# Performance work log

Hardware: AMD Instinct MI355X
Metric: run time of the kernel (lower is better)

The kernel has to match this reference:

```python
import jax, jax.numpy as jnp
import numpy as np

N_NODES = 50000
N_EDGES = 800000
IN_F = 128
OUT_F = 128
EDGE_F = 6


def setup_inputs() -> dict:
    key = jax.random.key(0)
    k1, k2, k3, k4, k5, k6, k7 = jax.random.split(key, 7)
    nodeFeatures = jax.random.normal(k1, (N_NODES, IN_F), dtype=jnp.float32)
    edgeIndex = jax.random.randint(k2, (N_EDGES, 2), 0, N_NODES, dtype=jnp.int64)
    edgeFeatures = jax.random.normal(k3, (N_EDGES, EDGE_F), dtype=jnp.float32)
    # nn.Linear params (kaiming-uniform-ish init scale)
    lim_n = 1.0 / np.sqrt(IN_F)
    lim_e = 1.0 / np.sqrt(EDGE_F)
    W = jax.random.uniform(k4, (IN_F, OUT_F), minval=-lim_n, maxval=lim_n, dtype=jnp.float32)
    b = jax.random.uniform(k5, (OUT_F,), minval=-lim_n, maxval=lim_n, dtype=jnp.float32)
    We = jax.random.uniform(k6, (EDGE_F, OUT_F), minval=-lim_e, maxval=lim_e, dtype=jnp.float32)
    be = jax.random.uniform(k7, (OUT_F,), minval=-lim_e, maxval=lim_e, dtype=jnp.float32)
    return {"nodeFeatures": nodeFeatures, "edgeIndex": edgeIndex,
            "edgeFeatures": edgeFeatures, "W": W, "b": b, "We": We, "be": be}


def reference(nodeFeatures, edgeIndex, edgeFeatures, W, b, We, be):
    # node linear: [N, out]
    transformed = nodeFeatures @ W + b
    # edge linear: [E, out]
    edgeMsg = edgeFeatures @ We + be
    src = edgeIndex[:, 0]
    dst = edgeIndex[:, 1]
    # per-edge message = transformed[src] + edgeMsg, scatter-add into dst
    messages = transformed[src] + edgeMsg  # [E, out]
    aggregated = jax.ops.segment_sum(messages, dst, num_segments=nodeFeatures.shape[0])
    return jax.nn.relu(aggregated)
```

## Files before the change

### kernel.cpp

```cpp
#include <hip/hip_runtime.h>
#include <hip/hip_bf16.h>
#include <stdint.h>

#define IN_F 128
#define EDGE_F 6
#define TILE_E 4096
#define NBIN_PAD 256
#define PADMAX 1792
#define K1_BLOCKS 2048

using bf16x8 = __attribute__((ext_vector_type(8))) short;
using f32x4  = __attribute__((ext_vector_type(4))) float;

__device__ __forceinline__ float bf2f(unsigned short u) {
    return __uint_as_float(((unsigned int)u) << 16);
}
__device__ __forceinline__ unsigned short f2bfbits(float f) {
    __hip_bfloat16 h = __float2bfloat16(f);
    return *reinterpret_cast<unsigned short*>(&h);
}
__device__ __forceinline__ unsigned int packbf(float a, float b) {
    return ((unsigned int)f2bfbits(b) << 16) | (unsigned int)f2bfbits(a);
}

__global__ __launch_bounds__(256) void hist_cast(
        const int* __restrict__ eidx, unsigned short* __restrict__ pmat,
        int n_edges, int nblk_e, int n_cast, int wblk, int n_nodes,
        const float* __restrict__ nf, unsigned short* __restrict__ nfb,
        const float* __restrict__ W, const float* __restrict__ b,
        const float* __restrict__ We, const float* __restrict__ be,
        unsigned short* __restrict__ Wpack, float* __restrict__ W2pack) {
    const int tid = threadIdx.x;
    const int blk = blockIdx.x;
    __shared__ int hist[NBIN_PAD];

    if (blk == wblk) {
        for (int idx = tid; idx < 16384; idx += 256) {
            int j = idx & 7, lane = (idx >> 3) & 63, ft = (idx >> 9) & 7, kb = idx >> 12;
            int k = kb * 32 + (lane >> 4) * 8 + j;
            int f = ft * 16 + (lane & 15);
            Wpack[idx] = f2bfbits(W[k * 128 + f]);
        }
        for (int idx = tid; idx < 1024; idx += 256) {
            int j = idx >> 7, f = idx & 127;
            float w = 0.f;
            if (j < 6)       w = We[j * 128 + f];
            else if (j == 6) w = b[f] + be[f];
            W2pack[idx] = w;
        }
        if (tid < 16) {
            uint4 z; z.x = z.y = z.z = z.w = 0u;
            reinterpret_cast<uint4*>(nfb + (size_t)n_nodes * IN_F)[tid] = z;
        }
    } else if (blk < nblk_e) {
        hist[tid] = 0;
        __syncthreads();
        const int e0 = blk * TILE_E;
#pragma unroll
        for (int i = 0; i < TILE_E / 256; ++i) {
            const int e = e0 + i * 256 + tid;
            if (e < n_edges) {
                const int dst = reinterpret_cast<const int2*>(eidx)[e].y;
                atomicAdd(&hist[dst >> 8], 1);
            }
        }
        __syncthreads();
        pmat[(size_t)blk * NBIN_PAD + tid] = (unsigned short)hist[tid];
    }
    const int t = blk * 256 + tid;
    const int stride = gridDim.x * 256;
    for (int i = t; i < n_cast; i += stride) {
        const float4 lo = reinterpret_cast<const float4*>(nf)[2 * i];
        const float4 hi = reinterpret_cast<const float4*>(nf)[2 * i + 1];
        uint4 o;
        o.x = packbf(lo.x, lo.y); o.y = packbf(lo.z, lo.w);
        o.z = packbf(hi.x, hi.y); o.w = packbf(hi.z, hi.w);
        reinterpret_cast<uint4*>(nfb)[i] = o;
    }
}

__global__ __launch_bounds__(256) void pack_scatter(
        const int* __restrict__ eidx, const float* __restrict__ ef,
        const unsigned short* __restrict__ pmat,
        uint4* __restrict__ rec_c, int* __restrict__ gbase,
        int n_edges, int nblk_e, int nbin) {
    const int tid = threadIdx.x;
    const int blk = blockIdx.x;
    __shared__ int cur[NBIN_PAD];
    __shared__ int sc[NBIN_PAD];
    int tot = 0, pre = 0;
#pragma unroll 4
    for (int bb = 0; bb < nblk_e; ++bb) {
        const int v = pmat[(size_t)bb * NBIN_PAD + tid];
        tot += v;
        pre += (bb < blk) ? v : 0;
    }
    sc[tid] = tot;
    __syncthreads();
    for (int off = 1; off < 256; off <<= 1) {
        int t2 = (tid >= off) ? sc[tid - off] : 0;
        __syncthreads();
        sc[tid] += t2;
        __syncthreads();
    }
    const int excl = sc[tid] - tot;
    cur[tid] = excl + pre;
    if (blk == 0 && tid <= nbin) gbase[tid] = excl;
    __syncthreads();
    const int e0 = blk * TILE_E;
#pragma unroll
    for (int i = 0; i < TILE_E / 256; ++i) {
        const int e = e0 + i * 256 + tid;
        if (e < n_edges) {
            const int2 pr = reinterpret_cast<const int2*>(eidx)[e];
            const float2* efs = reinterpret_cast<const float2*>(ef + (size_t)e * EDGE_F);
            const float2 f0 = efs[0], f1 = efs[1], f2 = efs[2];
            uint4 q;
            q.x = (unsigned int)pr.x | ((unsigned int)pr.y << 16);
            q.y = packbf(f0.x, f0.y);
            q.z = packbf(f1.x, f1.y);
            q.w = packbf(f2.x, f2.y);
            const int pos = atomicAdd(&cur[pr.y >> 8], 1);
            rec_c[pos] = q;
        }
    }
}

__global__ __launch_bounds__(256) void fine_rank(
        const uint4* __restrict__ rec_c, const int* __restrict__ gbase,
        uint4* __restrict__ rec, int2* __restrict__ pr2, int n_nodes) {
    const int tid = threadIdx.x;
    const int c = blockIdx.x;
    const int rbase = gbase[c], rend = gbase[c + 1];
    const int pbase = rbase + c * PADMAX;
    __shared__ int fcnt[256];
    __shared__ int fpos[256];
    fcnt[tid] = 0;
    __syncthreads();
    for (int i = rbase + tid; i < rend; i += 256) {
        const unsigned int qx = reinterpret_cast<const unsigned int*>(rec_c)[(size_t)i * 4];
        atomicAdd(&fcnt[(qx >> 16) & 255], 1);
    }
    __syncthreads();
    const int own = fcnt[tid];
    const int ownp = (own + 7) & ~7;
    fcnt[tid] = ownp;
    __syncthreads();
    for (int off = 1; off < 256; off <<= 1) {
        int t2 = (tid >= off) ? fcnt[tid - off] : 0;
        __syncthreads();
        fcnt[tid] += t2;
        __syncthreads();
    }
    const int pexcl = fcnt[tid] - ownp;
    fpos[tid] = pexcl;
    const int n = c * 256 + tid;
    if (n < n_nodes) {
        int2 pr; pr.x = pbase + pexcl; pr.y = own;
        pr2[n] = pr;
    }
    __syncthreads();
    for (int i = rbase + tid; i < rend; i += 256) {
        const uint4 q = rec_c[i];
        const int r = atomicAdd(&fpos[(q.x >> 16) & 255], 1);
        rec[pbase + r] = q;
    }
    uint4 dmy; dmy.x = (unsigned int)n_nodes; dmy.y = dmy.z = dmy.w = 0u;
    for (int j = own; j < ownp; ++j)
        rec[pbase + pexcl + j] = dmy;
}

__global__ __launch_bounds__(256) void aggregate_bf16(
        const unsigned short* __restrict__ nfb, const uint4* __restrict__ rec,
        const int2* __restrict__ pr2, unsigned short* __restrict__ S,
        unsigned short* __restrict__ E8, int n_nodes) {
    const int lane = threadIdx.x & 63;
    const int wv = __builtin_amdgcn_readfirstlane(threadIdx.x >> 6);
    const int n = blockIdx.x * 4 + wv;
    if (n >= n_nodes) return;
    const int2 pr = pr2[n];
    const int deg = pr.y;
    const int nb = (deg + 7) >> 3;
    const int half = lane >> 5;
    const int hl = lane & 31;
    float a0 = 0.f, a1 = 0.f, a2 = 0.f, a3 = 0.f;
    float e0 = 0.f, e1 = 0.f, e2 = 0.f, e3 = 0.f, e4 = 0.f, e5 = 0.f;
    int i = pr.x;
    for (int bb = 0; bb < nb; ++bb, i += 8) {
        uint4 q[8];
#pragma unroll
        for (int j = 0; j < 8; ++j) q[j] = rec[i + j];
        uint2 u[4];
#pragma unroll
        for (int p = 0; p < 4; ++p) {
            const unsigned int sA = q[2 * p].x & 0xFFFFu;
            const unsigned int sB = q[2 * p + 1].x & 0xFFFFu;
            const unsigned int s = half ? sB : sA;
            u[p] = reinterpret_cast<const uint2*>(nfb + (size_t)s * IN_F)[hl];
        }
#pragma unroll
        for (int p = 0; p < 4; ++p) {
            a0 += bf2f((unsigned short)u[p].x);
            a1 += bf2f((unsigned short)(u[p].x >> 16));
            a2 += bf2f((unsigned short)u[p].y);
            a3 += bf2f((unsigned short)(u[p].y >> 16));
        }
#pragma unroll
        for (int j = 0; j < 8; ++j) {
            e0 += bf2f((unsigned short)q[j].y);
            e1 += bf2f((unsigned short)(q[j].y >> 16));
            e2 += bf2f((unsigned short)q[j].z);
            e3 += bf2f((unsigned short)(q[j].z >> 16));
            e4 += bf2f((unsigned short)q[j].w);
            e5 += bf2f((unsigned short)(q[j].w >> 16));
        }
    }
    a0 += __shfl_xor(a0, 32, 64);
    a1 += __shfl_xor(a1, 32, 64);
    a2 += __shfl_xor(a2, 32, 64);
    a3 += __shfl_xor(a3, 32, 64);
    if (half == 0) {
        uint2 o;
        o.x = packbf(a0, a1);
        o.y = packbf(a2, a3);
        reinterpret_cast<uint2*>(S + (size_t)n * IN_F)[hl] = o;
    }
    if (lane == 0) {
        uint4 q;
        q.x = packbf(e0, e1);
        q.y = packbf(e2, e3);
        q.z = packbf(e4, e5);
        q.w = packbf((float)deg, 0.f);
        *reinterpret_cast<uint4*>(E8 + (size_t)n * 8) = q;
    }
}

__global__ __launch_bounds__(256) void gemm_mfma(
        const unsigned short* __restrict__ S, const unsigned short* __restrict__ E8,
        const unsigned short* __restrict__ Wpack, const float* __restrict__ W2pack,
        float* __restrict__ out, int n_nodes) {
    __shared__ __align__(16) short Wl[16384];
    __shared__ float W2l[1024];
    const int tid = threadIdx.x;
    for (int i = tid; i < 2048; i += 256)
        reinterpret_cast<uint4*>(Wl)[i] = reinterpret_cast<const uint4*>(Wpack)[i];
    for (int i = tid; i < 1024; i += 256) W2l[i] = W2pack[i];

    const int wv = tid >> 6, lane = tid & 63;
    const int m = lane & 15, quad = lane >> 4;
    const int n0 = blockIdx.x * 64 + wv * 16;

    const int arow = min(n0 + m, n_nodes - 1);
    const unsigned short* ap = S + (size_t)arow * IN_F + quad * 8;
    bf16x8 a[4];
#pragma unroll
    for (int kb = 0; kb < 4; ++kb)
        a[kb] = *reinterpret_cast<const bf16x8*>(ap + kb * 32);

    __syncthreads();

    f32x4 acc[8];
#pragma unroll
    for (int ft = 0; ft < 8; ++ft) acc[ft] = (f32x4){0.f, 0.f, 0.f, 0.f};

#pragma unroll
    for (int kb = 0; kb < 4; ++kb) {
#pragma unroll
        for (int ft = 0; ft < 8; ++ft) {
            const bf16x8 bfrag =
                reinterpret_cast<const bf16x8*>(Wl)[(kb * 8 + ft) * 64 + lane];
            acc[ft] = __builtin_amdgcn_mfma_f32_16x16x32_bf16(a[kb], bfrag, acc[ft], 0, 0, 0);
        }
    }

    float e[4][7];
#pragma unroll
    for (int r = 0; r < 4; ++r) {
        const int n = min(n0 + quad * 4 + r, n_nodes - 1);
        const uint4 q = *reinterpret_cast<const uint4*>(E8 + (size_t)n * 8);
        e[r][0] = bf2f((unsigned short)q.x); e[r][1] = bf2f((unsigned short)(q.x >> 16));
        e[r][2] = bf2f((unsigned short)q.y); e[r][3] = bf2f((unsigned short)(q.y >> 16));
        e[r][4] = bf2f((unsigned short)q.z); e[r][5] = bf2f((unsigned short)(q.z >> 16));
        e[r][6] = bf2f((unsigned short)q.w);
    }
#pragma unroll
    for (int ft = 0; ft < 8; ++ft) {
        const int f = ft * 16 + m;
        float w2[7];
#pragma unroll
        for (int j = 0; j < 7; ++j) w2[j] = W2l[j * 128 + f];
#pragma unroll
        for (int r = 0; r < 4; ++r) {
            const int n = n0 + quad * 4 + r;
            if (n < n_nodes) {
                float v = acc[ft][r];
#pragma unroll
                for (int j = 0; j < 7; ++j) v += e[r][j] * w2[j];
                out[(size_t)n * 128 + f] = fmaxf(v, 0.f);
            }
        }
    }
}

extern "C" void kernel_launch(void* const* d_in, const int* in_sizes, int n_in,
                              void* d_out, int out_size, void* d_ws, size_t ws_size,
                              hipStream_t stream) {
    const float* nf = (const float*)d_in[0];
    const int* eidx = (const int*)d_in[1];
    const float* ef = (const float*)d_in[2];
    const float* W  = (const float*)d_in[3];
    const float* b  = (const float*)d_in[4];
    const float* We = (const float*)d_in[5];
    const float* be = (const float*)d_in[6];
    float* out = (float*)d_out;

    const int n_nodes = in_sizes[0] / IN_F;
    const int n_edges = in_sizes[1] / 2;

    const int nblk_e = (n_edges + TILE_E - 1) / TILE_E;
    const int nbin = (n_nodes + 255) >> 8;
    const int n_cast = n_nodes * (IN_F / 8);

    uint4* rec   = (uint4*)d_ws;
    uint4* rec_c = rec + ((size_t)n_edges + (size_t)nbin * PADMAX);
    unsigned short* S = (unsigned short*)(rec_c + n_edges);
    unsigned short* E8 = S + (size_t)n_nodes * IN_F;
    unsigned short* Wpack = E8 + (size_t)n_nodes * 8;
    float* W2pack = (float*)(Wpack + 16384);
    unsigned short* pmat = (unsigned short*)(W2pack + 1024);
    int* gbase = (int*)(pmat + (size_t)nblk_e * NBIN_PAD);
    int2* pr2 = (int2*)(gbase + 260);
    unsigned short* nfb = (unsigned short*)(pr2 + n_nodes);

    hist_cast<<<K1_BLOCKS + 1, 256, 0, stream>>>(eidx, pmat,
                                                 n_edges, nblk_e, n_cast, K1_BLOCKS,
                                                 n_nodes, nf, nfb,
                                                 W, b, We, be, Wpack, W2pack);
    pack_scatter<<<nblk_e, 256, 0, stream>>>(eidx, ef, pmat, rec_c, gbase,
                                             n_edges, nblk_e, nbin);
    fine_rank<<<nbin, 256, 0, stream>>>(rec_c, gbase, rec, pr2, n_nodes);
    aggregate_bf16<<<(n_nodes + 3) / 4, 256, 0, stream>>>(nfb, rec, pr2, S, E8, n_nodes);
    gemm_mfma<<<(n_nodes + 63) / 64, 256, 0, stream>>>(S, E8, Wpack, W2pack, out, n_nodes);
}
```

Measured before the change: 196.8 us.

## Fuse histogram and scatter into per-tile local sort, gather runs in fine_rank

Replaces the global two-pass counting sort (histogram kernel, then a scatter kernel with a full prefix scan over all tile histograms) with a single kernel in which each edge tile does a local bucket sort into its own segment and records per-bin counts and offsets. fine_rank then reads each bin's runs directly from every tile's segment using those offsets, writing into fixed-capacity per-bin output slots (BCAP). This removes one kernel launch and a full extra read of the edge index. The cost is strided gathers from many small runs in fine_rank, and records are silently dropped if a bin ever exceeds BCAP edges.

After: 195.4 us. About the same (-0.7%).

```diff
diff --git a/kernel.cpp b/kernel.cpp
--- a/kernel.cpp
+++ b/kernel.cpp
@@ -6,8 +6,8 @@
 #define EDGE_F 6
 #define TILE_E 4096
 #define NBIN_PAD 256
-#define PADMAX 1792
-#define K1_BLOCKS 2048
+#define BCAP 8192
+#define CAST_B 400
 
 using bf16x8 = __attribute__((ext_vector_type(8))) short;
 using f32x4  = __attribute__((ext_vector_type(4))) float;
@@ -23,18 +23,59 @@
     return ((unsigned int)f2bfbits(b) << 16) | (unsigned int)f2bfbits(a);
 }
 
-__global__ __launch_bounds__(256) void hist_cast(
-        const int* __restrict__ eidx, unsigned short* __restrict__ pmat,
-        int n_edges, int nblk_e, int n_cast, int wblk, int n_nodes,
+__global__ __launch_bounds__(256) void sort_pack_cast(
+        const int* __restrict__ eidx, const float* __restrict__ ef,
+        uint4* __restrict__ rec_c, unsigned short* __restrict__ pmat,
+        unsigned short* __restrict__ lmat,
+        int n_edges, int nblk_e, int n_cast, int n_nodes,
         const float* __restrict__ nf, unsigned short* __restrict__ nfb,
         const float* __restrict__ W, const float* __restrict__ b,
         const float* __restrict__ We, const float* __restrict__ be,
         unsigned short* __restrict__ Wpack, float* __restrict__ W2pack) {
     const int tid = threadIdx.x;
     const int blk = blockIdx.x;
+    __shared__ unsigned int qxs[TILE_E];
     __shared__ int hist[NBIN_PAD];
-
-    if (blk == wblk) {
+    __shared__ int cur[NBIN_PAD];
+
+    if (blk < nblk_e) {
+        hist[tid] = 0;
+        __syncthreads();
+        const int e0 = blk * TILE_E;
+        const int lim = min(TILE_E, n_edges - e0);
+        for (int i = tid; i < lim; i += 256) {
+            const int2 pr = reinterpret_cast<const int2*>(eidx)[e0 + i];
+            const unsigned int q = (unsigned int)pr.x | ((unsigned int)pr.y << 16);
+            qxs[i] = q;
+            atomicAdd(&hist[q >> 24], 1);
+        }
+        __syncthreads();
+        const int own = hist[tid];
+        for (int off = 1; off < 256; off <<= 1) {
+            int t2 = (tid >= off) ? hist[tid - off] : 0;
+            __syncthreads();
+            hist[tid] += t2;
+            __syncthreads();
+        }
+        const int excl = hist[tid] - own;
+        pmat[(size_t)blk * NBIN_PAD + tid] = (unsigned short)own;
+        lmat[(size_t)blk * NBIN_PAD + tid] = (unsigned short)excl;
+        cur[tid] = excl;
+        __syncthreads();
+        uint4* seg = rec_c + (size_t)blk * TILE_E;
+        for (int i = tid; i < lim; i += 256) {
+            const unsigned int q = qxs[i];
+            const float2* efs = reinterpret_cast<const float2*>(ef + (size_t)(e0 + i) * EDGE_F);
+            const float2 f0 = efs[0], f1 = efs[1], f2 = efs[2];
+            uint4 r;
+            r.x = q;
+            r.y = packbf(f0.x, f0.y);
+            r.z = packbf(f1.x, f1.y);
+            r.w = packbf(f2.x, f2.y);
+            const int pos = atomicAdd(&cur[q >> 24], 1);
+            seg[pos] = r;
+        }
+    } else if (blk == nblk_e) {
         for (int idx = tid; idx < 16384; idx += 256) {
             int j = idx & 7, lane = (idx >> 3) & 63, ft = (idx >> 9) & 7, kb = idx >> 12;
             int k = kb * 32 + (lane >> 4) * 8 + j;
@@ -52,93 +93,36 @@
             uint4 z; z.x = z.y = z.z = z.w = 0u;
             reinterpret_cast<uint4*>(nfb + (size_t)n_nodes * IN_F)[tid] = z;
         }
-    } else if (blk < nblk_e) {
-        hist[tid] = 0;
-        __syncthreads();
-        const int e0 = blk * TILE_E;
-#pragma unroll
-        for (int i = 0; i < TILE_E / 256; ++i) {
-            const int e = e0 + i * 256 + tid;
-            if (e < n_edges) {
-                const int dst = reinterpret_cast<const int2*>(eidx)[e].y;
-                atomicAdd(&hist[dst >> 8], 1);
-            }
-        }
-        __syncthreads();
-        pmat[(size_t)blk * NBIN_PAD + tid] = (unsigned short)hist[tid];
-    }
-    const int t = blk * 256 + tid;
-    const int stride = gridDim.x * 256;
-    for (int i = t; i < n_cast; i += stride) {
-        const float4 lo = reinterpret_cast<const float4*>(nf)[2 * i];
-        const float4 hi = reinterpret_cast<const float4*>(nf)[2 * i + 1];
-        uint4 o;
-        o.x = packbf(lo.x, lo.y); o.y = packbf(lo.z, lo.w);
-        o.z = packbf(hi.x, hi.y); o.w = packbf(hi.z, hi.w);
-        reinterpret_cast<uint4*>(nfb)[i] = o;
-    }
-}
-
-__global__ __launch_bounds__(256) void pack_scatter(
-        const int* __restrict__ eidx, const float* __restrict__ ef,
-        const unsigned short* __restrict__ pmat,
-        uint4* __restrict__ rec_c, int* __restrict__ gbase,
-        int n_edges, int nblk_e, int nbin) {
-    const int tid = threadIdx.x;
-    const int blk = blockIdx.x;
-    __shared__ int cur[NBIN_PAD];
-    __shared__ int sc[NBIN_PAD];
-    int tot = 0, pre = 0;
-#pragma unroll 4
-    for (int bb = 0; bb < nblk_e; ++bb) {
-        const int v = pmat[(size_t)bb * NBIN_PAD + tid];
-        tot += v;
-        pre += (bb < blk) ? v : 0;
-    }
-    sc[tid] = tot;
-    __syncthreads();
-    for (int off = 1; off < 256; off <<= 1) {
-        int t2 = (tid >= off) ? sc[tid - off] : 0;
-        __syncthreads();
-        sc[tid] += t2;
-        __syncthreads();
-    }
-    const int excl = sc[tid] - tot;
-    cur[tid] = excl + pre;
-    if (blk == 0 && tid <= nbin) gbase[tid] = excl;
-    __syncthreads();
-    const int e0 = blk * TILE_E;
-#pragma unroll
-    for (int i = 0; i < TILE_E / 256; ++i) {
-        const int e = e0 + i * 256 + tid;
-        if (e < n_edges) {
-            const int2 pr = reinterpret_cast<const int2*>(eidx)[e];
-            const float2* efs = reinterpret_cast<const float2*>(ef + (size_t)e * EDGE_F);
-            const float2 f0 = efs[0], f1 = efs[1], f2 = efs[2];
-            uint4 q;
-            q.x = (unsigned int)pr.x | ((unsigned int)pr.y << 16);
-            q.y = packbf(f0.x, f0.y);
-            q.z = packbf(f1.x, f1.y);
-            q.w = packbf(f2.x, f2.y);
-            const int pos = atomicAdd(&cur[pr.y >> 8], 1);
-            rec_c[pos] = q;
+    } else {
+        const int cb = blk - nblk_e - 1;
+        const int ncb = gridDim.x - nblk_e - 1;
+        for (int i = cb * 256 + tid; i < n_cast; i += ncb * 256) {
+            const float4 lo = reinterpret_cast<const float4*>(nf)[2 * i];
+            const float4 hi = reinterpret_cast<const float4*>(nf)[2 * i + 1];
+            uint4 o;
+            o.x = packbf(lo.x, lo.y); o.y = packbf(lo.z, lo.w);
+            o.z = packbf(hi.x, hi.y); o.w = packbf(hi.z, hi.w);
+            reinterpret_cast<uint4*>(nfb)[i] = o;
         }
     }
 }
 
 __global__ __launch_bounds__(256) void fine_rank(
-        const uint4* __restrict__ rec_c, const int* __restrict__ gbase,
-        uint4* __restrict__ rec, int2* __restrict__ pr2, int n_nodes) {
+        const uint4* __restrict__ rec_c, const unsigned short* __restrict__ pmat,
+        const unsigned short* __restrict__ lmat,
+        uint4* __restrict__ rec, int2* __restrict__ pr2,
+        int n_nodes, int nblk_e) {
     const int tid = threadIdx.x;
     const int c = blockIdx.x;
-    const int rbase = gbase[c], rend = gbase[c + 1];
-    const int pbase = rbase + c * PADMAX;
     __shared__ int fcnt[256];
     __shared__ int fpos[256];
+    const int cnt_t = (tid < nblk_e) ? pmat[(size_t)tid * NBIN_PAD + c] : 0;
+    const int ofs_t = (tid < nblk_e) ? lmat[(size_t)tid * NBIN_PAD + c] : 0;
+    const uint4* runp = rec_c + (size_t)tid * TILE_E + ofs_t;
     fcnt[tid] = 0;
     __syncthreads();
-    for (int i = rbase + tid; i < rend; i += 256) {
-        const unsigned int qx = reinterpret_cast<const unsigned int*>(rec_c)[(size_t)i * 4];
+    for (int k = 0; k < cnt_t; ++k) {
+        const unsigned int qx = reinterpret_cast<const unsigned int*>(runp)[4 * k];
         atomicAdd(&fcnt[(qx >> 16) & 255], 1);
     }
     __syncthreads();
@@ -154,20 +138,21 @@
     }
     const int pexcl = fcnt[tid] - ownp;
     fpos[tid] = pexcl;
+    const size_t obase = (size_t)c * BCAP;
     const int n = c * 256 + tid;
     if (n < n_nodes) {
-        int2 pr; pr.x = pbase + pexcl; pr.y = own;
+        int2 pr; pr.x = (int)(obase + pexcl); pr.y = own;
         pr2[n] = pr;
     }
     __syncthreads();
-    for (int i = rbase + tid; i < rend; i += 256) {
-        const uint4 q = rec_c[i];
+    for (int k = 0; k < cnt_t; ++k) {
+        const uint4 q = runp[k];
         const int r = atomicAdd(&fpos[(q.x >> 16) & 255], 1);
-        rec[pbase + r] = q;
+        if (r < BCAP) rec[obase + r] = q;
     }
     uint4 dmy; dmy.x = (unsigned int)n_nodes; dmy.y = dmy.z = dmy.w = 0u;
-    for (int j = own; j < ownp; ++j)
-        rec[pbase + pexcl + j] = dmy;
+    for (int j = own; j < ownp && pexcl + j < BCAP; ++j)
+        rec[obase + pexcl + j] = dmy;
 }
 
 __global__ __launch_bounds__(256) void aggregate_bf16(
@@ -322,23 +307,21 @@
     const int n_cast = n_nodes * (IN_F / 8);
 
     uint4* rec   = (uint4*)d_ws;
-    uint4* rec_c = rec + ((size_t)n_edges + (size_t)nbin * PADMAX);
-    unsigned short* S = (unsigned short*)(rec_c + n_edges);
+    uint4* rec_c = rec + (size_t)nbin * BCAP;
+    unsigned short* S = (unsigned short*)(rec_c + (size_t)nblk_e * TILE_E);
     unsigned short* E8 = S + (size_t)n_nodes * IN_F;
     unsigned short* Wpack = E8 + (size_t)n_nodes * 8;
     float* W2pack = (float*)(Wpack + 16384);
-    unsigned short* pmat = (unsigned short*)(W2pack + 1024);
-    int* gbase = (int*)(pmat + (size_t)nblk_e * NBIN_PAD);
-    int2* pr2 = (int2*)(gbase + 260);
-    unsigned short* nfb = (unsigned short*)(pr2 + n_nodes);
-
-    hist_cast<<<K1_BLOCKS + 1, 256, 0, stream>>>(eidx, pmat,
-                                                 n_edges, nblk_e, n_cast, K1_BLOCKS,
-                                                 n_nodes, nf, nfb,
-                                                 W, b, We, be, Wpack, W2pack);
-    pack_scatter<<<nblk_e, 256, 0, stream>>>(eidx, ef, pmat, rec_c, gbase,
-                                             n_edges, nblk_e, nbin);
-    fine_rank<<<nbin, 256, 0, stream>>>(rec_c, gbase, rec, pr2, n_nodes);
+    int2* pr2 = (int2*)(W2pack + 1024);
+    unsigned short* pmat = (unsigned short*)(pr2 + n_nodes);
+    unsigned short* lmat = pmat + (size_t)nblk_e * NBIN_PAD;
+    unsigned short* nfb = lmat + (size_t)nblk_e * NBIN_PAD;
+
+    sort_pack_cast<<<nblk_e + 1 + CAST_B, 256, 0, stream>>>(
+        eidx, ef, rec_c, pmat, lmat, n_edges, nblk_e, n_cast, n_nodes,
+        nf, nfb, W, b, We, be, Wpack, W2pack);
+    fine_rank<<<nbin, 256, 0, stream>>>(rec_c, pmat, lmat, rec, pr2,
+                                        n_nodes, nblk_e);
     aggregate_bf16<<<(n_nodes + 3) / 4, 256, 0, stream>>>(nfb, rec, pr2, S, E8, n_nodes);
     gemm_mfma<<<(n_nodes + 63) / 64, 256, 0, stream>>>(S, E8, Wpack, W2pack, out, n_nodes);
 }
```
